# Performance work log

Hardware: AMD Instinct MI355X
Metric: run time of the kernel (lower is better)

## Reference

```python
import jax, jax.numpy as jnp
import numpy as np

K = 9        # kernel_size (neighbors)
GROUPS = 4   # BasicConv uses nn.Conv2d(..., groups=4)


def setup_inputs() -> dict:
    key = jax.random.key(0)
    k1, k2 = jax.random.split(key, 2)
    x = jax.random.normal(k1, (8, 192, 56, 56), dtype=jnp.float32)
    # grouped 1x1 conv: weight (out_channels, 2*in_channels/groups) = (384, 96)
    fan_in = 2 * 192 // GROUPS
    W = jax.random.normal(k2, (384, fan_in), dtype=jnp.float32) * (2.0 / fan_in) ** 0.5
    b = jnp.zeros((384,), dtype=jnp.float32)
    return {"x": x, "W": W, "b": b}


def _knn_idx(xf, k):
    # xf: (B, C, N). L2-normalize channels (F.normalize dim=1), squared euclid dist.
    xn = xf / jnp.maximum(jnp.linalg.norm(xf, axis=1, keepdims=True), 1e-12)
    pts = jnp.transpose(xn, (0, 2, 1))                  # (B, N, C)
    sq = jnp.sum(pts * pts, axis=-1)                    # (B, N)
    dist = sq[:, :, None] - 2.0 * jnp.einsum('bnc,bmc->bnm', pts, pts) + sq[:, None, :]
    _, nn_idx = jax.lax.top_k(-dist, k)                 # (B, N, k) smallest distances
    return nn_idx


def reference(x, W, b):
    B, C, H, Wd = x.shape
    N = H * Wd
    xf = x.reshape(B, C, N)                             # flatten spatial -> graph nodes
    nn_idx = _knn_idx(jax.lax.stop_gradient(xf), K)     # knn built under no_grad in torch
    # gather neighbor features: x_j[b,c,n,k] = xf[b,c,nn_idx[b,n,k]]
    x_j = jax.vmap(lambda f, idx: f[:, idx])(xf, nn_idx)   # (B, C, N, K)
    x_i = jnp.broadcast_to(xf[:, :, :, None], x_j.shape)   # center features
    feat = jnp.concatenate([x_i, x_j - x_i], axis=1)       # (B, 2C, N, K)
    # grouped 1x1 conv (groups=4) + bias + relu
    Cin, Cout = feat.shape[1], W.shape[0]
    fg = feat.reshape(B, GROUPS, Cin // GROUPS, N, K)
    Wg = W.reshape(GROUPS, Cout // GROUPS, Cin // GROUPS)
    out = jnp.einsum('bgcnk,goc->bgonk', fg, Wg).reshape(B, Cout, N, K)
    out = jax.nn.relu(out + b[None, :, None, None])
    out = jnp.max(out, axis=-1)                         # max-aggregate over neighbors
    return out.reshape(B, Cout, H, Wd)
```

## Files before the change

### kernel.cpp

```cpp
#include <hip/hip_runtime.h>
#include <hip/hip_bf16.h>
#include <cstdint>

#define B_ 8
#define C_ 192
#define N_ 3136
#define K_ 9
#define OC_ 384
#define QT_ 49
#define MS_ 4
#define NT_ 25
#define QSZ 24576

typedef unsigned int u32;
typedef _Float16 f16x8 __attribute__((ext_vector_type(8)));
typedef __fp16 h2 __attribute__((ext_vector_type(2)));
typedef float f32x4 __attribute__((ext_vector_type(4)));

#define GLD(g, s) __builtin_amdgcn_global_load_lds( \
    (const __attribute__((address_space(1))) void*)(g), \
    (__attribute__((address_space(3))) void*)(s), 16, 0, 0)

#define WAITV4 asm volatile("s_waitcnt vmcnt(4)" ::: "memory")
#define WAITV0 asm volatile("s_waitcnt vmcnt(0)" ::: "memory")

#define INS(LV, LI, dd, mm) { \
    float cv = (dd); int ci = (mm); \
    _Pragma("unroll") \
    for (int r_ = 0; r_ < 9; ++r_) { \
        bool sw_ = cv < LV[r_]; \
        float tv_ = LV[r_]; int ti_ = LI[r_]; \
        LV[r_] = sw_ ? cv : tv_;  LI[r_] = sw_ ? ci : ti_; \
        cv = sw_ ? tv_ : cv;      ci = sw_ ? ti_ : ci; \
    } }

__global__ __launch_bounds__(64) void prep_k(const float* __restrict__ x,
                                             _Float16* __restrict__ pHL,
                                             float* __restrict__ xT,
                                             float* __restrict__ sq) {
    int g = blockIdx.x * 64 + threadIdx.x;
    int b = g / N_, n = g % N_;
    const float* xb = x + (size_t)b * C_ * N_ + n;
    float ss = 0.f;
    for (int c = 0; c < C_; ++c) { float v = xb[(size_t)c * N_]; ss = fmaf(v, v, ss); }
    float den = fmaxf(sqrtf(ss), 1e-12f);
    float* xrow = xT + (size_t)g * C_;
    _Float16* hrow = pHL + (size_t)g * 384;
    float s2 = 0.f;
    for (int c4 = 0; c4 < 48; ++c4) {
        float4 vv; float* pv = &vv.x;
        union { _Float16 f[4]; uint2 u; } uh, ul;
        #pragma unroll
        for (int j = 0; j < 4; ++j) {
            int c = 4 * c4 + j;
            float v = xb[(size_t)c * N_];
            float p = v / den;
            pv[j] = v;
            _Float16 h = (_Float16)p;
            uh.f[j] = h;
            ul.f[j] = (_Float16)(p - (float)h);
            s2 = fmaf(p, p, s2);
        }
        *(float4*)&xrow[4 * c4] = vv;
        *(uint2*)&hrow[4 * c4] = uh.u;
        *(uint2*)&hrow[192 + 4 * c4] = ul.u;
    }
    sq[g] = s2;
}

__global__ __launch_bounds__(256, 2) void knn_k(const _Float16* __restrict__ pHL,
                                                const float* __restrict__ sq,
                                                float* __restrict__ pkv,
                                                int* __restrict__ pki) {
    __shared__ _Float16 sh[40960];
    float* dist = (float*)(sh + QSZ + 8192);
    const int tid = threadIdx.x;
    const int w = tid >> 6, l = tid & 63;
    const int lr = l & 15, lg = l >> 4;
    const int bid = blockIdx.x;
    const int b = bid & 7;
    const int r2_ = bid >> 3;
    const int qt = r2_ >> 2, s4 = r2_ & 3;
    const int q0 = qt * 64;
    const char* hbB = (const char*)(pHL + (size_t)b * N_ * 384);
    const float* sqb = sq + b * N_;

    const int nl = l >> 3, sl = l & 7, ol = sl ^ nl;
    const size_t lane_src = (size_t)nl * 768 + (size_t)(ol >> 2) * 384 + (size_t)(ol & 3) * 16;
    const int slot_h = (lg ^ (lr & 7)) * 8;
    const int slot_l = ((4 | lg) ^ (lr & 7)) * 8;

    float sqq[4][4];
    #pragma unroll
    for (int qs = 0; qs < 4; ++qs)
        #pragma unroll
        for (int r = 0; r < 4; ++r) sqq[qs][r] = sqb[q0 + 16 * qs + 4 * lg + r];

    float lvA[9], lvB[9]; int liA[9], liB[9];
    #pragma unroll
    for (int r = 0; r < 9; ++r) {
        lvA[r] = INFINITY; liA[r] = 0x7fffffff;
        lvB[r] = INFINITY; liB[r] = 0x7fffffff;
    }

    auto stageM = [&](int mt_, int kc_, int buf) {
        size_t mb = (size_t)(mt_ * 128 + w * 32) * 768 + (size_t)kc_ * 64;
        _Float16* md = sh + QSZ + buf * 8192 + w * 2048;
        #pragma unroll
        for (int i = 0; i < 4; ++i)
            GLD(hbB + mb + (size_t)i * 6144 + lane_src, md + i * 512);
    };

    #pragma unroll
    for (int kc = 0; kc < 6; ++kc) {
        size_t qb = (size_t)(q0 + w * 16) * 768 + (size_t)kc * 64;
        _Float16* qd = sh + kc * 4096 + w * 1024;
        GLD(hbB + qb + lane_src, qd);
        GLD(hbB + qb + 6144 + lane_src, qd + 512);
    }
    __syncthreads();
    stageM(s4, 0, 0);

    for (int mt = s4; mt < NT_; mt += MS_) {
        const int m0 = mt * 128;
        f32x4 acc[4][2];
        #pragma unroll
        for (int qs = 0; qs < 4; ++qs)
            #pragma unroll
            for (int ms = 0; ms < 2; ++ms) acc[qs][ms] = (f32x4)0.f;

        #pragma unroll
        for (int kc = 0; kc < 6; ++kc) {
            const int nmt = (kc < 5) ? mt : mt + MS_;
            const int nkc = (kc < 5) ? kc + 1 : 0;
            if (nmt < NT_) {
                stageM(nmt, nkc, (kc + 1) & 1);
                WAITV4;
            } else {
                WAITV0;
            }
            const _Float16* Qb = sh + kc * 4096;
            const _Float16* Mb = sh + QSZ + (kc & 1) * 8192;
            f16x8 ah[4], al[4];
            #pragma unroll
            for (int qs = 0; qs < 4; ++qs) {
                const _Float16* qrow = Qb + (16 * qs + lr) * 64;
                ah[qs] = *(const f16x8*)(qrow + slot_h);
                al[qs] = *(const f16x8*)(qrow + slot_l);
            }
            #pragma unroll
            for (int ms = 0; ms < 2; ++ms) {
                const _Float16* mrow = Mb + (32 * w + 16 * ms + lr) * 64;
                f16x8 bh = *(const f16x8*)(mrow + slot_h);
                f16x8 bl = *(const f16x8*)(mrow + slot_l);
                #pragma unroll
                for (int qs = 0; qs < 4; ++qs) {
                    acc[qs][ms] = __builtin_amdgcn_mfma_f32_16x16x32_f16(al[qs], bh, acc[qs][ms], 0, 0, 0);
                    acc[qs][ms] = __builtin_amdgcn_mfma_f32_16x16x32_f16(ah[qs], bl, acc[qs][ms], 0, 0, 0);
                    acc[qs][ms] = __builtin_amdgcn_mfma_f32_16x16x32_f16(ah[qs], bh, acc[qs][ms], 0, 0, 0);
                }
            }
        }
        __syncthreads();

        float sqm[2];
        #pragma unroll
        for (int ms = 0; ms < 2; ++ms) {
            int m = m0 + 32 * w + 16 * ms + lr;
            sqm[ms] = (m < N_) ? sqb[m] : 0.f;
        }
        #pragma unroll
        for (int pm = 0; pm < 2; ++pm) {
            if (m0 + 64 * pm >= N_) break;
            if ((w >> 1) == pm) {
                #pragma unroll
                for (int qs = 0; qs < 4; ++qs)
                    #pragma unroll
                    for (int ms = 0; ms < 2; ++ms) {
                        int col = 32 * (w & 1) + 16 * ms + lr;
                        int gsw = ((4 * qs + lg) ^ lr) << 2;
                        float4 v;
                        v.x = (sqq[qs][0] - 2.0f * acc[qs][ms][0]) + sqm[ms];
                        v.y = (sqq[qs][1] - 2.0f * acc[qs][ms][1]) + sqm[ms];
                        v.z = (sqq[qs][2] - 2.0f * acc[qs][ms][2]) + sqm[ms];
                        v.w = (sqq[qs][3] - 2.0f * acc[qs][ms][3]) + sqm[ms];
                        *(float4*)&dist[col * 64 + gsw] = v;
                    }
            }
            __syncthreads();
            const int gq = l >> 2, qe = l & 3;
            #pragma unroll
            for (int jj = 0; jj < 16; ++jj) {
                int col = 16 * w + jj;
                int m = m0 + 64 * pm + col;
                if (m < N_) {
                    float d = dist[col * 64 + ((gq ^ (col & 15)) << 2) + qe];
                    if (jj & 1) { INS(lvB, liB, d, m) }
                    else        { INS(lvA, liA, d, m) }
                }
            }
            __syncthreads();
        }
    }
    float* Lv = (float*)sh;
    int*   Li = (int*)sh + 4608;
    #pragma unroll
    for (int r = 0; r < 9; ++r) {
        Lv[(tid * 2 + 0) * 9 + r] = lvA[r]; Li[(tid * 2 + 0) * 9 + r] = liA[r];
        Lv[(tid * 2 + 1) * 9 + r] = lvB[r]; Li[(tid * 2 + 1) * 9 + r] = liB[r];
    }
    __syncthreads();
    if (tid < 64) {
        size_t base = ((size_t)((b * QT_ + qt) * MS_ + s4) * 64 + tid) * 9;
        for (int r = 0; r < K_; ++r) {
            float best = INFINITY; int bidx = 0x7fffffff; int bp = 0;
            for (int s = 0; s < 8; ++s) {
                int lb = (((s >> 1) * 64 + tid) * 2 + (s & 1)) * 9;
                for (int e = 0; e < 9; ++e) {
                    float v = Lv[lb + e]; int id = Li[lb + e];
                    if (v < best || (v == best && id < bidx)) { best = v; bidx = id; bp = lb + e; }
                }
            }
            pkv[base + r] = best;
            pki[base + r] = bidx;
            Lv[bp] = INFINITY;
        }
    }
}

__global__ __launch_bounds__(64) void merge_k(const float* __restrict__ pkv,
                                              const int* __restrict__ pki,
                                              int* __restrict__ nn) {
    int g = blockIdx.x * 64 + threadIdx.x;
    int b = g / N_, n = g % N_;
    int qt = n >> 6, q = n & 63;
    float v[MS_ * 9]; int id[MS_ * 9];
    #pragma unroll
    for (int s = 0; s < MS_; ++s) {
        size_t base = ((size_t)((b * QT_ + qt) * MS_ + s) * 64 + q) * 9;
        #pragma unroll
        for (int e = 0; e < 9; ++e) { v[s * 9 + e] = pkv[base + e]; id[s * 9 + e] = pki[base + e]; }
    }
    int* onn = nn + (size_t)g * K_;
    for (int r = 0; r < K_; ++r) {
        float best = INFINITY; int bidx = 0x7fffffff; int bp = 0;
        #pragma unroll
        for (int e = 0; e < MS_ * 9; ++e) {
            if (v[e] < best || (v[e] == best && id[e] < bidx)) { best = v[e]; bidx = id[e]; bp = e; }
        }
        onn[r] = bidx;
        v[bp] = INFINITY;
    }
}

__global__ __launch_bounds__(256) void convi_k(const float* __restrict__ x,
                                               const float* __restrict__ W,
                                               const float* __restrict__ bias,
                                               float* __restrict__ out) {
    __shared__ float Ws[24 * 96];
    const int orange = blockIdx.x & 7;
    const int nb = blockIdx.x >> 3;
    const int tid = threadIdx.x;
    const int g = nb * 256 + tid;
    const int b = g / N_, n = g % N_;
    const int o0 = orange * 24;
    const int cb = (o0 >= 96) ? 96 : 0;
    for (int i = 0; i < 9; ++i) {
        int e = tid + i * 256;
        Ws[e] = W[o0 * 96 + e];
    }
    __syncthreads();
    const float* xb = x + ((size_t)b * C_ + cb) * N_ + n;
    float xi[96];
    #pragma unroll
    for (int c = 0; c < 96; ++c) xi[c] = xb[(size_t)c * N_];
    float* ob = out + ((size_t)b * OC_ + o0) * N_ + n;
    for (int o = 0; o < 24; ++o) {
        float a = bias[o0 + o];
        #pragma unroll
        for (int c4 = 0; c4 < 24; ++c4) {
            float4 w4 = *(const float4*)&Ws[o * 96 + 4 * c4];
            a = fmaf(w4.x, xi[4*c4+0], a);
            a = fmaf(w4.y, xi[4*c4+1], a);
            a = fmaf(w4.z, xi[4*c4+2], a);
            a = fmaf(w4.w, xi[4*c4+3], a);
        }
        ob[(size_t)o * N_] = fmaxf(a, 0.f);
    }
}

__global__ __launch_bounds__(256) void convd_k(const float* __restrict__ xT,
                                               const int* __restrict__ nn,
                                               const float* __restrict__ W,
                                               const float* __restrict__ bias,
                                               float* __restrict__ out) {
    __shared__ _Float16 Wb[192 * 106];
    __shared__ _Float16 dif[4][9 * 192];
    const int tid = threadIdx.x;
    const int w = tid >> 6, l = tid & 63;
    const int b = blockIdx.x / 196;
    const int n0 = (blockIdx.x % 196) * 16;
    const bool hi2 = (l >= 32);

    for (int i = 0; i < 72; ++i) {
        int e = tid + i * 256;
        int row = e / 96, j = e % 96;
        Wb[row * 106 + j] = (_Float16)W[(192 + row) * 96 + j];
    }
    float bo[3];
    #pragma unroll
    for (int oi = 0; oi < 3; ++oi) bo[oi] = bias[192 + l + 64 * oi];
    __syncthreads();

    _Float16* df = dif[w];
    const float* xTb = xT + (size_t)b * N_ * C_;
    float mx0[4], mx1[4], mx2[4];

    #pragma unroll
    for (int r = 0; r < 4; ++r) {
        const int n = n0 + 4 * w + r;
        const float* xin = xTb + (size_t)n * C_;
        float xi0 = xin[l], xi1 = xin[l + 64], xi2 = xin[l + 128];
        const int* nb2 = nn + ((size_t)b * N_ + n) * K_;
        __syncthreads();
        #pragma unroll
        for (int k = 0; k < K_; ++k) {
            int idx = nb2[k];
            const float* xj = xTb + (size_t)idx * C_;
            df[k * 192 + l]       = (_Float16)(xj[l]       - xi0);
            df[k * 192 + l + 64]  = (_Float16)(xj[l + 64]  - xi1);
            df[k * 192 + l + 128] = (_Float16)(xj[l + 128] - xi2);
        }
        __syncthreads();
        float a0[9], a1[9], a2[9];
        #pragma unroll
        for (int k = 0; k < 9; ++k) { a0[k] = 0.f; a1[k] = 0.f; a2[k] = 0.f; }

        for (int jj = 0; jj < 12; ++jj) {
            union U { uint4 u; h2 p[4]; };
            U w0u, w1u, w2u;
            w0u.u = *(const uint4*)(Wb + (size_t)l * 106 + jj * 8);
            w1u.u = *(const uint4*)(Wb + (size_t)(l + 64) * 106 + jj * 8);
            w2u.u = *(const uint4*)(Wb + (size_t)(l + 128) * 106 + jj * 8);
            #pragma unroll
            for (int k = 0; k < 9; ++k) {
                const _Float16* dk = df + k * 192 + jj * 8;
                U dA, dB, dC;
                dA.u = *(const uint4*)(dk);
                dB.u = *(const uint4*)(dk + 96);
                dC.u.x = hi2 ? dB.u.x : dA.u.x;
                dC.u.y = hi2 ? dB.u.y : dA.u.y;
                dC.u.z = hi2 ? dB.u.z : dA.u.z;
                dC.u.w = hi2 ? dB.u.w : dA.u.w;
                #pragma unroll
                for (int p = 0; p < 4; ++p) {
                    a0[k] = __builtin_amdgcn_fdot2(w0u.p[p], dA.p[p], a0[k], false);
                    a1[k] = __builtin_amdgcn_fdot2(w1u.p[p], dC.p[p], a1[k], false);
                    a2[k] = __builtin_amdgcn_fdot2(w2u.p[p], dB.p[p], a2[k], false);
                }
            }
        }
        float m0 = a0[0] + bo[0], m1 = a1[0] + bo[1], m2 = a2[0] + bo[2];
        #pragma unroll
        for (int k = 1; k < 9; ++k) {
            m0 = fmaxf(m0, a0[k] + bo[0]);
            m1 = fmaxf(m1, a1[k] + bo[1]);
            m2 = fmaxf(m2, a2[k] + bo[2]);
        }
        mx0[r] = fmaxf(m0, 0.f); mx1[r] = fmaxf(m1, 0.f); mx2[r] = fmaxf(m2, 0.f);
    }
    float* ob = out + ((size_t)b * OC_ + 192) * N_ + n0 + 4 * w;
    *(float4*)&ob[(size_t)(l)       * N_] = make_float4(mx0[0], mx0[1], mx0[2], mx0[3]);
    *(float4*)&ob[(size_t)(l + 64)  * N_] = make_float4(mx1[0], mx1[1], mx1[2], mx1[3]);
    *(float4*)&ob[(size_t)(l + 128) * N_] = make_float4(mx2[0], mx2[1], mx2[2], mx2[3]);
}

extern "C" void kernel_launch(void* const* d_in, const int* in_sizes, int n_in,
                              void* d_out, int out_size, void* d_ws, size_t ws_size,
                              hipStream_t stream) {
    (void)in_sizes; (void)n_in; (void)out_size; (void)ws_size;
    const float* x    = (const float*)d_in[0];
    const float* W    = (const float*)d_in[1];
    const float* bias = (const float*)d_in[2];
    float* out = (float*)d_out;

    _Float16* pHL = (_Float16*)d_ws;
    float* xT   = (float*)(pHL + (size_t)B_ * N_ * 384);
    float* sq   = xT + (size_t)B_ * N_ * C_;
    int*   nn   = (int*)(sq + (size_t)B_ * N_);
    float* pkv  = (float*)(nn + (size_t)B_ * N_ * K_);
    int*   pki  = (int*)(pkv + (size_t)B_ * QT_ * MS_ * 64 * 9);

    hipLaunchKernelGGL(prep_k,  dim3(392),  dim3(64),  0, stream, x, pHL, xT, sq);
    hipLaunchKernelGGL(knn_k,   dim3(B_ * QT_ * MS_), dim3(256), 0, stream, pHL, sq, pkv, pki);
    hipLaunchKernelGGL(merge_k, dim3(392),  dim3(64),  0, stream, pkv, pki, nn);
    hipLaunchKernelGGL(convi_k, dim3(784),  dim3(256), 0, stream, x, W, bias, out);
    hipLaunchKernelGGL(convd_k, dim3(1568), dim3(256), 0, stream, xT, nn, W, bias, out);
}
```

Measured before the change: 795.1 us.

## Shrink KNN key tile to 64 columns and drop cross-tile prefetch

Key tiles in the KNN distance kernel shrink from 128 to 64 columns, so each wave computes one 16-column MFMA slice instead of two. LDS drops from 80KB to 64KB, and the boundary checks go away because 3136 divides evenly by 64. Staging of the next key tile is no longer prefetched across mt iterations; each tile now starts with an unoverlapped first load. Each Q fragment load now feeds half as many MFMAs, and the per-tile barrier and top-k insert phases run twice as often.

```diff
diff --git a/kernel.cpp b/kernel.cpp
--- a/kernel.cpp
+++ b/kernel.cpp
@@ -9,7 +9,7 @@
 #define OC_ 384
 #define QT_ 49
 #define MS_ 4
-#define NT_ 25
+#define NT_ 49
 #define QSZ 24576
 
 typedef unsigned int u32;
@@ -21,7 +21,7 @@
     (const __attribute__((address_space(1))) void*)(g), \
     (__attribute__((address_space(3))) void*)(s), 16, 0, 0)
 
-#define WAITV4 asm volatile("s_waitcnt vmcnt(4)" ::: "memory")
+#define WAITV2 asm volatile("s_waitcnt vmcnt(2)" ::: "memory")
 #define WAITV0 asm volatile("s_waitcnt vmcnt(0)" ::: "memory")
 
 #define INS(LV, LI, dd, mm) { \
@@ -72,8 +72,8 @@
                                                 const float* __restrict__ sq,
                                                 float* __restrict__ pkv,
                                                 int* __restrict__ pki) {
-    __shared__ _Float16 sh[40960];
-    float* dist = (float*)(sh + QSZ + 8192);
+    __shared__ _Float16 sh[32768];
+    float* dist = (float*)(sh + QSZ);
     const int tid = threadIdx.x;
     const int w = tid >> 6, l = tid & 63;
     const int lr = l & 15, lg = l >> 4;
@@ -104,11 +104,10 @@
     }
 
     auto stageM = [&](int mt_, int kc_, int buf) {
-        size_t mb = (size_t)(mt_ * 128 + w * 32) * 768 + (size_t)kc_ * 64;
-        _Float16* md = sh + QSZ + buf * 8192 + w * 2048;
-        #pragma unroll
-        for (int i = 0; i < 4; ++i)
-            GLD(hbB + mb + (size_t)i * 6144 + lane_src, md + i * 512);
+        size_t mb = (size_t)(mt_ * 64 + w * 16) * 768 + (size_t)kc_ * 64;
+        _Float16* md = sh + QSZ + buf * 4096 + w * 1024;
+        GLD(hbB + mb + lane_src, md);
+        GLD(hbB + mb + 6144 + lane_src, md + 512);
     };
 
     #pragma unroll
@@ -119,88 +118,63 @@
         GLD(hbB + qb + 6144 + lane_src, qd + 512);
     }
     __syncthreads();
-    stageM(s4, 0, 0);
 
     for (int mt = s4; mt < NT_; mt += MS_) {
-        const int m0 = mt * 128;
-        f32x4 acc[4][2];
-        #pragma unroll
-        for (int qs = 0; qs < 4; ++qs)
-            #pragma unroll
-            for (int ms = 0; ms < 2; ++ms) acc[qs][ms] = (f32x4)0.f;
+        const int m0 = mt * 64;
+        stageM(mt, 0, 0);
+        f32x4 acc[4];
+        #pragma unroll
+        for (int qs = 0; qs < 4; ++qs) acc[qs] = (f32x4)0.f;
 
         #pragma unroll
         for (int kc = 0; kc < 6; ++kc) {
-            const int nmt = (kc < 5) ? mt : mt + MS_;
-            const int nkc = (kc < 5) ? kc + 1 : 0;
-            if (nmt < NT_) {
-                stageM(nmt, nkc, (kc + 1) & 1);
-                WAITV4;
+            if (kc < 5) {
+                stageM(mt, kc + 1, (kc + 1) & 1);
+                WAITV2;
             } else {
                 WAITV0;
             }
             const _Float16* Qb = sh + kc * 4096;
-            const _Float16* Mb = sh + QSZ + (kc & 1) * 8192;
-            f16x8 ah[4], al[4];
+            const _Float16* mrow = sh + QSZ + (kc & 1) * 4096 + (16 * w + lr) * 64;
+            f16x8 bh = *(const f16x8*)(mrow + slot_h);
+            f16x8 bl = *(const f16x8*)(mrow + slot_l);
             #pragma unroll
             for (int qs = 0; qs < 4; ++qs) {
                 const _Float16* qrow = Qb + (16 * qs + lr) * 64;
-                ah[qs] = *(const f16x8*)(qrow + slot_h);
-                al[qs] = *(const f16x8*)(qrow + slot_l);
-            }
+                f16x8 ah = *(const f16x8*)(qrow + slot_h);
+                f16x8 al = *(const f16x8*)(qrow + slot_l);
+                acc[qs] = __builtin_amdgcn_mfma_f32_16x16x32_f16(al, bh, acc[qs], 0, 0, 0);
+                acc[qs] = __builtin_amdgcn_mfma_f32_16x16x32_f16(ah, bl, acc[qs], 0, 0, 0);
+                acc[qs] = __builtin_amdgcn_mfma_f32_16x16x32_f16(ah, bh, acc[qs], 0, 0, 0);
+            }
+        }
+        __syncthreads();
+
+        const float sqm = sqb[m0 + 16 * w + lr];
+        {
+            const int col = 16 * w + lr;
             #pragma unroll
-            for (int ms = 0; ms < 2; ++ms) {
-                const _Float16* mrow = Mb + (32 * w + 16 * ms + lr) * 64;
-                f16x8 bh = *(const f16x8*)(mrow + slot_h);
-                f16x8 bl = *(const f16x8*)(mrow + slot_l);
-                #pragma unroll
-                for (int qs = 0; qs < 4; ++qs) {
-                    acc[qs][ms] = __builtin_amdgcn_mfma_f32_16x16x32_f16(al[qs], bh, acc[qs][ms], 0, 0, 0);
-                    acc[qs][ms] = __builtin_amdgcn_mfma_f32_16x16x32_f16(ah[qs], bl, acc[qs][ms], 0, 0, 0);
-                    acc[qs][ms] = __builtin_amdgcn_mfma_f32_16x16x32_f16(ah[qs], bh, acc[qs][ms], 0, 0, 0);
-                }
-            }
-        }
-        __syncthreads();
-
-        float sqm[2];
-        #pragma unroll
-        for (int ms = 0; ms < 2; ++ms) {
-            int m = m0 + 32 * w + 16 * ms + lr;
-            sqm[ms] = (m < N_) ? sqb[m] : 0.f;
-        }
-        #pragma unroll
-        for (int pm = 0; pm < 2; ++pm) {
-            if (m0 + 64 * pm >= N_) break;
-            if ((w >> 1) == pm) {
-                #pragma unroll
-                for (int qs = 0; qs < 4; ++qs)
-                    #pragma unroll
-                    for (int ms = 0; ms < 2; ++ms) {
-                        int col = 32 * (w & 1) + 16 * ms + lr;
-                        int gsw = ((4 * qs + lg) ^ lr) << 2;
-                        float4 v;
-                        v.x = (sqq[qs][0] - 2.0f * acc[qs][ms][0]) + sqm[ms];
-                        v.y = (sqq[qs][1] - 2.0f * acc[qs][ms][1]) + sqm[ms];
-                        v.z = (sqq[qs][2] - 2.0f * acc[qs][ms][2]) + sqm[ms];
-                        v.w = (sqq[qs][3] - 2.0f * acc[qs][ms][3]) + sqm[ms];
-                        *(float4*)&dist[col * 64 + gsw] = v;
-                    }
-            }
-            __syncthreads();
-            const int gq = l >> 2, qe = l & 3;
-            #pragma unroll
-            for (int jj = 0; jj < 16; ++jj) {
-                int col = 16 * w + jj;
-                int m = m0 + 64 * pm + col;
-                if (m < N_) {
-                    float d = dist[col * 64 + ((gq ^ (col & 15)) << 2) + qe];
-                    if (jj & 1) { INS(lvB, liB, d, m) }
-                    else        { INS(lvA, liA, d, m) }
-                }
-            }
-            __syncthreads();
-        }
+            for (int qs = 0; qs < 4; ++qs) {
+                int gsw = ((4 * qs + lg) ^ lr) << 2;
+                float4 v;
+                v.x = (sqq[qs][0] - 2.0f * acc[qs][0]) + sqm;
+                v.y = (sqq[qs][1] - 2.0f * acc[qs][1]) + sqm;
+                v.z = (sqq[qs][2] - 2.0f * acc[qs][2]) + sqm;
+                v.w = (sqq[qs][3] - 2.0f * acc[qs][3]) + sqm;
+                *(float4*)&dist[col * 64 + gsw] = v;
+            }
+        }
+        __syncthreads();
+        const int gq = l >> 2, qe = l & 3;
+        #pragma unroll
+        for (int jj = 0; jj < 16; ++jj) {
+            int col = 16 * w + jj;
+            int m = m0 + col;
+            float d = dist[col * 64 + ((gq ^ (col & 15)) << 2) + qe];
+            if (jj & 1) { INS(lvB, liB, d, m) }
+            else        { INS(lvA, liA, d, m) }
+        }
+        __syncthreads();
     }
     float* Lv = (float*)sh;
     int*   Li = (int*)sh + 4608;
```

Measured after the change: 673.9 us. 15.2% less time.
